# Kernel optimization log

Hardware: AMD Instinct MI355X
Metric: run time of the kernel (lower is better)

## Reference

```python
import jax, jax.numpy as jnp
import numpy as np

EMBED = 1024
HEADS = 16
HEAD_DIM = EMBED // HEADS
EPS = 1e-5  # torch LayerNorm default


def setup_inputs() -> dict:
    key = jax.random.key(0)
    ks = jax.random.split(key, 11)
    s = 1.0 / np.sqrt(EMBED)
    def lin(kw, kb):
        W = jax.random.uniform(kw, (EMBED, EMBED), jnp.float32, -s, s)
        b = jax.random.uniform(kb, (EMBED,), jnp.float32, -s, s)
        return W, b
    Wq, bq = lin(ks[0], ks[1])
    Wk, bk = lin(ks[2], ks[3])
    Wv, bv = lin(ks[4], ks[5])
    Wo, bo = lin(ks[6], ks[7])
    x = jax.random.normal(ks[8], (2, 2048, EMBED), jnp.float32)
    gamma = jnp.ones((EMBED,), jnp.float32)
    beta = jnp.zeros((EMBED,), jnp.float32)
    return {"x": x, "Wq": Wq, "bq": bq, "Wk": Wk, "bk": bk,
            "Wv": Wv, "bv": bv, "Wo": Wo, "bo": bo,
            "gamma": gamma, "beta": beta}


def _attn(x, Wq, bq, Wk, bk, Wv, bv, Wo, bo, gamma, beta):
    N, S, _ = x.shape
    # torch Linear: y = x @ W.T + b
    q = (x @ Wq.T + bq).reshape(N, S, HEADS, HEAD_DIM).transpose(0, 2, 1, 3)
    k = (x @ Wk.T + bk).reshape(N, S, HEADS, HEAD_DIM).transpose(0, 2, 1, 3)
    v = (x @ Wv.T + bv).reshape(N, S, HEADS, HEAD_DIM).transpose(0, 2, 1, 3)
    energy = jnp.einsum("bhqd,bhkd->bhqk", q, k) / np.sqrt(HEAD_DIM)
    causal = jnp.tril(jnp.ones((S, S), bool))  # [S,S]
    energy = jnp.where(causal[None, None], energy, -jnp.inf)
    attn = jax.nn.softmax(energy, axis=-1)
    out = jnp.einsum("bhqk,bhkd->bhqd", attn, v)
    out = out.transpose(0, 2, 1, 3).reshape(N, S, EMBED)
    out = out @ Wo.T + bo
    # residual + LayerNorm
    h = out + x
    mu = jnp.mean(h, axis=-1, keepdims=True)
    var = jnp.var(h, axis=-1, keepdims=True)
    return (h - mu) * jax.lax.rsqrt(var + EPS) * gamma + beta


def reference(x, Wq, bq, Wk, bk, Wv, bv, Wo, bo, gamma, beta):
    return _attn(x, Wq, bq, Wk, bk, Wv, bv, Wo, bo, gamma, beta)
```

## Files before the change

### kernel.cpp

```cpp
#include <hip/hip_runtime.h>

typedef __attribute__((ext_vector_type(8))) short short8;
typedef __attribute__((ext_vector_type(4))) float f32x4;
typedef __attribute__((ext_vector_type(4))) short short4v;

template<bool B> struct BoolC { static constexpr bool value = B; };

__device__ __forceinline__ short f2bs(float f) {
    union { float f; unsigned u; } c; c.f = f;
    unsigned r = 0x7FFFu + ((c.u >> 16) & 1u);
    return (short)((c.u + r) >> 16);
}

__device__ __forceinline__ float bs2f(short s) {
    union { unsigned u; float f; } c; c.u = ((unsigned)(unsigned short)s) << 16;
    return c.f;
}

__device__ __forceinline__ unsigned fbits(float f) {
    union { float f; unsigned u; } c; c.f = f; return c.u;
}

__device__ __forceinline__ float fast_exp2(float x) {
    float r;
    asm("v_exp_f32 %0, %1" : "=v"(r) : "v"(x));
    return r;
}

__device__ __forceinline__ void gld_lds16(const void* g, void* l) {
    __builtin_amdgcn_global_load_lds(
        (const __attribute__((address_space(1))) unsigned int*)g,
        (__attribute__((address_space(3))) unsigned int*)l, 16, 0, 0);
}

__device__ __forceinline__ f32x4 mfma16(short8 a, short8 b, f32x4 c) {
    return __builtin_amdgcn_mfma_f32_16x16x32_bf16(a, b, c, 0, 0, 0);
}

template<int N> __device__ __forceinline__ void vmwait() {
    if constexpr (N == 0)      asm volatile("s_waitcnt vmcnt(0)" ::: "memory");
    else if constexpr (N == 3) asm volatile("s_waitcnt vmcnt(3)" ::: "memory");
    else if constexpr (N == 4) asm volatile("s_waitcnt vmcnt(4)" ::: "memory");
}

__global__ __launch_bounds__(256) void cvtall_kernel(
    const float* __restrict__ x,
    const float* __restrict__ Wq, const float* __restrict__ Wk,
    const float* __restrict__ Wv, const float* __restrict__ Wo,
    short* __restrict__ xb, short* __restrict__ wqkv, short* __restrict__ wob)
{
    int i = blockIdx.x * 256 + threadIdx.x;
    const float* src; short* dst; int off;
    if (i < 1048576) { src = x; dst = xb; off = i; }
    else {
        int j = i - 1048576, which = j >> 18;
        off = j & 262143;
        src = which == 0 ? Wq : (which == 1 ? Wk : (which == 2 ? Wv : Wo));
        dst = which == 3 ? wob : (wqkv + (size_t)which * 1048576);
    }
    float4 v = ((const float4*)src)[off];
    short4v o;
    o.x = f2bs(v.x); o.y = f2bs(v.y); o.z = f2bs(v.z); o.w = f2bs(v.w);
    ((short4v*)dst)[off] = o;
}

#define BK 32

template<int MODE, int BMt, int BNt, int NTHR>
__global__ __launch_bounds__(NTHR) void gemm_bt(
    const short* __restrict__ A, const short* __restrict__ B,
    int M, int N, int K,
    const float* __restrict__ b0, const float* __restrict__ b1, const float* __restrict__ b2,
    short* __restrict__ oq, short* __restrict__ ok_, short* __restrict__ ov,
    const float* __restrict__ bo, const float* __restrict__ xres,
    short* __restrict__ outh)
{
    constexpr int WCOLS = BNt / 64;
    constexpr int IM = BMt / 2 / 16;
    constexpr int BUFSZ = (BMt + BNt) * BK;
    __shared__ __align__(16) short SM[3 * BUFSZ];
    const int tid = threadIdx.x;
    const int wave = tid >> 6, lane = tid & 63;
    const int lhi = lane >> 4, llo = lane & 15;
    const int row0 = blockIdx.x * BMt, col0 = blockIdx.y * BNt;
    const int wr = (wave / WCOLS) * (BMt / 2);
    const int wc = (wave % WCOLS) * 64;

    f32x4 acc[IM][4] = {};

    const short* gA0 = A + (size_t)(row0 + (tid >> 2)) * K + (tid & 3) * 8;
    const short* gB0 = B + (size_t)(col0 + (tid >> 2)) * K + (tid & 3) * 8;
    const short* gB1 = B + (size_t)(col0 + NTHR / 4 + (tid >> 2)) * K + (tid & 3) * 8;

    auto stage = [&](int kk, int bf) {
        short* As = SM + bf * BUFSZ;
        short* Bs = As + BMt * BK;
        gld_lds16(gA0 + kk, &As[wave * 512]);
        gld_lds16(gB0 + kk, &Bs[wave * 512]);
        gld_lds16(gB1 + kk, &Bs[NTHR * 8 + wave * 512]);
    };

    const int NT = K / BK;
    stage(0, 0);
    stage(BK, 1);

    for (int kt = 0; kt < NT; ++kt) {
        if (kt < NT - 1) vmwait<3>(); else vmwait<0>();
        __builtin_amdgcn_s_barrier();
        __builtin_amdgcn_sched_barrier(0);
        if (kt + 2 < NT) stage((kt + 2) * BK, (kt + 2) % 3);
        const short* As = SM + (kt % 3) * BUFSZ;
        const short* Bs = As + BMt * BK;
        short8 af[IM], bfr[4];
        #pragma unroll
        for (int i = 0; i < IM; ++i)
            af[i] = *(const short8*)&As[(wr + i * 16 + llo) * BK + lhi * 8];
        #pragma unroll
        for (int j = 0; j < 4; ++j)
            bfr[j] = *(const short8*)&Bs[(wc + j * 16 + llo) * BK + lhi * 8];
        #pragma unroll
        for (int i = 0; i < IM; ++i)
            #pragma unroll
            for (int j = 0; j < 4; ++j)
                acc[i][j] = mfma16(af[i], bfr[j], acc[i][j]);
    }

    if constexpr (MODE == 0) {
        const int which = col0 >> 10;
        if (which < 2) {
            const float* bia = which == 0 ? b0 : b1;
            short* dst = which == 0 ? oq : ok_;
            #pragma unroll
            for (int i = 0; i < IM; ++i)
                #pragma unroll
                for (int j = 0; j < 4; ++j)
                    #pragma unroll
                    for (int r = 0; r < 4; ++r) {
                        int m = row0 + wr + i * 16 + lhi * 4 + r;
                        int nn = (col0 & 1023) + wc + j * 16 + llo;
                        float v = acc[i][j][r] + bia[nn];
                        int h = nn >> 6, d = nn & 63;
                        int bb = m >> 11, s = m & 2047;
                        dst[((size_t)((bb * 16 + h) * 2048 + s)) * 64 + d] = f2bs(v);
                    }
        } else {
            __syncthreads();
            short* T = SM + wave * (64 * 26);
            const int nn0 = (col0 - 2048) + wc;
            const int h = nn0 >> 6;
            const int bb = row0 >> 11;
            const int s0 = (row0 & 2047) + wr;
            short* vdst = ov + ((size_t)(bb * 16 + h) * 64) * 2048;
            #pragma unroll
            for (int i = 0; i < IM; ++i) {
                #pragma unroll
                for (int j = 0; j < 4; ++j) {
                    const float bias = b2[nn0 + j * 16 + llo];
                    unsigned u01 = __builtin_amdgcn_perm(fbits(acc[i][j][1] + bias),
                                                         fbits(acc[i][j][0] + bias), 0x07060302u);
                    unsigned u23 = __builtin_amdgcn_perm(fbits(acc[i][j][3] + bias),
                                                         fbits(acc[i][j][2] + bias), 0x07060302u);
                    unsigned* Tw = (unsigned*)&T[(j * 16 + llo) * 26];
                    Tw[lhi * 2]     = u01;
                    Tw[lhi * 2 + 1] = u23;
                }
                short8 a0 = *(const short8*)&T[lane * 26];
                short8 a1 = *(const short8*)&T[lane * 26 + 8];
                *(short8*)&vdst[(size_t)lane * 2048 + s0 + i * 16]     = a0;
                *(short8*)&vdst[(size_t)lane * 2048 + s0 + i * 16 + 8] = a1;
            }
        }
    } else {
        #pragma unroll
        for (int i = 0; i < IM; ++i)
            #pragma unroll
            for (int j = 0; j < 4; ++j)
                #pragma unroll
                for (int r = 0; r < 4; ++r) {
                    int m = row0 + wr + i * 16 + lhi * 4 + r;
                    int n = col0 + wc + j * 16 + llo;
                    size_t idx = (size_t)m * N + n;
                    outh[idx] = f2bs(acc[i][j][r] + bo[n] + xres[idx]);
                }
    }
}

#define SCL 0.18033688011f

__global__ __launch_bounds__(256) void attn_kernel(
    const short* __restrict__ Q, const short* __restrict__ K,
    const short* __restrict__ Vt, short* __restrict__ O)
{
    const int id = blockIdx.x;
    const int u = id >> 3;
    const int bh = (id & 7) * 4 + (u & 3);
    const int s4 = u >> 2;
    const int p = (s4 < 8) ? (2 * s4) : (31 - 2 * s4);
    const int q0L = p * 64, q0H = (31 - p) * 64;
    const int ntH = 32 - p;

    const short* Qb = Q  + (size_t)bh * 2048 * 64;
    const short* Kb = K  + (size_t)bh * 2048 * 64;
    const short* Vb = Vt + (size_t)bh * 64 * 2048;

    __shared__ __align__(16) short Ks[2][64 * 64];
    __shared__ __align__(16) short Vs[2][64 * 64];
    __shared__ __align__(16) short Ps[4][2][16 * 68];

    const int tid = threadIdx.x, wave = tid >> 6, lane = tid & 63;
    const int lhi = lane >> 4, llo = lane & 15;
    const int qwL = q0L + wave * 16, qwH = q0H + wave * 16;
    const int qgL = qwL + llo, qgH = qwH + llo;

    auto scale8 = [](short8 a) {
        short8 r;
        #pragma unroll
        for (int i = 0; i < 8; ++i) {
            union { unsigned u; float f; } c; c.u = ((unsigned)(unsigned short)a[i]) << 16;
            r[i] = f2bs(c.f * SCL);
        }
        return r;
    };
    const short8 qfL0 = scale8(*(const short8*)&Qb[(size_t)(qwL + llo) * 64 + lhi * 8]);
    const short8 qfL1 = scale8(*(const short8*)&Qb[(size_t)(qwL + llo) * 64 + 32 + lhi * 8]);
    const short8 qfH0 = scale8(*(const short8*)&Qb[(size_t)(qwH + llo) * 64 + lhi * 8]);
    const short8 qfH1 = scale8(*(const short8*)&Qb[(size_t)(qwH + llo) * 64 + 32 + lhi * 8]);

    const int tr = tid >> 3, tc = tid & 7, sc = tc ^ (tr & 7);
    const short* kS0 = Kb + (size_t)tr * 64 + sc * 8;
    const short* kS1 = Kb + (size_t)(32 + tr) * 64 + sc * 8;
    const short* vS0 = Vb + (size_t)tr * 2048 + sc * 8;
    const short* vS1 = Vb + (size_t)(32 + tr) * 2048 + sc * 8;
    const int dOff = wave * 512;

    f32x4 oL[4] = {}, oH[4] = {};
    float lL = 0.f, lH = 0.f;

    unsigned* PwH = (unsigned*)Ps[wave][0] + llo * 34;
    unsigned* PwL = (unsigned*)Ps[wave][1] + llo * 34;

    gld_lds16(kS0, Ks[0] + dOff);
    gld_lds16(kS1, Ks[0] + 2048 + dOff);
    gld_lds16(vS0, Vs[0] + dOff);
    gld_lds16(vS1, Vs[0] + 2048 + dOff);
    __syncthreads();

    const int swq = (llo & 7) << 3;

    auto smx = [&](f32x4 (&st)[4], float& lrow, unsigned* Pw, int qg, int kk0, bool diag) {
        if (diag) {
            #pragma unroll
            for (int t = 0; t < 4; ++t)
                #pragma unroll
                for (int j = 0; j < 4; ++j)
                    if (kk0 + t * 16 + lhi * 4 + j > qg) st[t][j] = -1e30f;
        }
        float rs0 = 0.f, rs1 = 0.f;
        #pragma unroll
        for (int t = 0; t < 4; ++t) {
            st[t][0] = fast_exp2(st[t][0]);
            st[t][1] = fast_exp2(st[t][1]);
            st[t][2] = fast_exp2(st[t][2]);
            st[t][3] = fast_exp2(st[t][3]);
            rs0 += st[t][0] + st[t][2];
            rs1 += st[t][1] + st[t][3];
        }
        lrow += rs0 + rs1;
        #pragma unroll
        for (int t = 0; t < 4; ++t) {
            uint2 w;
            w.x = __builtin_amdgcn_perm(fbits(st[t][1]), fbits(st[t][0]), 0x07060302u);
            w.y = __builtin_amdgcn_perm(fbits(st[t][3]), fbits(st[t][2]), 0x07060302u);
            *(uint2*)&Pw[t * 8 + lhi * 2] = w;
        }
    };

    int cur = 0;
    auto tile = [&](int kt, auto dualc) {
        constexpr bool DUAL = decltype(dualc)::value;
        const int kk0 = kt * 64;
        if (kt + 1 < ntH) {
            const int nk = kk0 + 64;
            gld_lds16(kS0 + (size_t)nk * 64, Ks[cur ^ 1] + dOff);
            gld_lds16(kS1 + (size_t)nk * 64, Ks[cur ^ 1] + 2048 + dOff);
            gld_lds16(vS0 + nk, Vs[cur ^ 1] + dOff);
            gld_lds16(vS1 + nk, Vs[cur ^ 1] + 2048 + dOff);
        }

        f32x4 stH[4], stL[4];
        __builtin_amdgcn_s_setprio(1);
        #pragma unroll
        for (int t = 0; t < 4; ++t) {
            const int row = t * 16 + llo;
            short8 kf0 = *(const short8*)&Ks[cur][row * 64 + ((lhi * 8) ^ swq)];
            short8 kf1 = *(const short8*)&Ks[cur][row * 64 + ((lhi * 8 + 32) ^ swq)];
            f32x4 a = {};
            a = mfma16(kf0, qfH0, a);
            stH[t] = mfma16(kf1, qfH1, a);
            if (DUAL) {
                f32x4 b = {};
                b = mfma16(kf0, qfL0, b);
                stL[t] = mfma16(kf1, qfL1, b);
            }
        }
        __builtin_amdgcn_s_setprio(0);

        smx(stH, lH, PwH, qgH, kk0, kt == ntH - 1);
        if (DUAL) smx(stL, lL, PwL, qgL, kk0, kt == p);

        const short8 pH0 = *(const short8*)&Ps[wave][0][llo * 68 + lhi * 8];
        const short8 pH1 = *(const short8*)&Ps[wave][0][llo * 68 + 32 + lhi * 8];
        short8 pL0, pL1;
        if (DUAL) {
            pL0 = *(const short8*)&Ps[wave][1][llo * 68 + lhi * 8];
            pL1 = *(const short8*)&Ps[wave][1][llo * 68 + 32 + lhi * 8];
        }
        __builtin_amdgcn_s_setprio(1);
        #pragma unroll
        for (int dt = 0; dt < 4; ++dt) {
            const int row = dt * 16 + llo;
            short8 vf0 = *(const short8*)&Vs[cur][row * 64 + ((lhi * 8) ^ swq)];
            short8 vf1 = *(const short8*)&Vs[cur][row * 64 + ((lhi * 8 + 32) ^ swq)];
            oH[dt] = mfma16(pH0, vf0, oH[dt]);
            oH[dt] = mfma16(pH1, vf1, oH[dt]);
            if (DUAL) {
                oL[dt] = mfma16(pL0, vf0, oL[dt]);
                oL[dt] = mfma16(pL1, vf1, oL[dt]);
            }
        }
        __builtin_amdgcn_s_setprio(0);

        if (kt + 1 < ntH) __syncthreads();
        cur ^= 1;
    };

    for (int kt = 0; kt <= p; ++kt)      tile(kt, BoolC<true>{});
    for (int kt = p + 1; kt < ntH; ++kt) tile(kt, BoolC<false>{});

    lH += __shfl_xor(lH, 16); lH += __shfl_xor(lH, 32);
    lL += __shfl_xor(lL, 16); lL += __shfl_xor(lL, 32);
    const int b = bh >> 4, h = bh & 15;
    const float invH = 1.f / lH, invL = 1.f / lL;
    #pragma unroll
    for (int j = 0; j < 4; ++j) {
        const float ivH = __shfl(invH, lhi * 4 + j);
        const float ivL = __shfl(invL, lhi * 4 + j);
        const size_t rowH = (size_t)(b * 2048 + qwH + lhi * 4 + j);
        const size_t rowL = (size_t)(b * 2048 + qwL + lhi * 4 + j);
        #pragma unroll
        for (int dt = 0; dt < 4; ++dt) {
            int d = dt * 16 + llo;
            O[rowH * 1024 + h * 64 + d] = f2bs(oH[dt][j] * ivH);
            O[rowL * 1024 + h * 64 + d] = f2bs(oL[dt][j] * ivL);
        }
    }
}

__global__ __launch_bounds__(256) void ln_kernel(const short* __restrict__ hb,
        float* __restrict__ out,
        const float* __restrict__ gamma, const float* __restrict__ beta)
{
    const int row = blockIdx.x;
    const short* pin = hb + (size_t)row * 1024;
    float* pout = out + (size_t)row * 1024;
    const int tid = threadIdx.x;
    short4v hv = ((const short4v*)pin)[tid];
    float4 v;
    v.x = bs2f(hv.x); v.y = bs2f(hv.y); v.z = bs2f(hv.z); v.w = bs2f(hv.w);
    float s = v.x + v.y + v.z + v.w;
    float ss = v.x * v.x + v.y * v.y + v.z * v.z + v.w * v.w;
    #pragma unroll
    for (int d = 1; d < 64; d <<= 1) {
        s  += __shfl_xor(s, d);
        ss += __shfl_xor(ss, d);
    }
    __shared__ float red[8];
    const int wave = tid >> 6, lane = tid & 63;
    if (lane == 0) { red[wave] = s; red[4 + wave] = ss; }
    __syncthreads();
    s  = red[0] + red[1] + red[2] + red[3];
    ss = red[4] + red[5] + red[6] + red[7];
    const float mu = s * (1.0f / 1024.0f);
    const float var = ss * (1.0f / 1024.0f) - mu * mu;
    const float rstd = rsqrtf(var + 1e-5f);
    float4 g = ((const float4*)gamma)[tid];
    float4 b = ((const float4*)beta)[tid];
    v.x = (v.x - mu) * rstd * g.x + b.x;
    v.y = (v.y - mu) * rstd * g.y + b.y;
    v.z = (v.z - mu) * rstd * g.z + b.z;
    v.w = (v.w - mu) * rstd * g.w + b.w;
    ((float4*)pout)[tid] = v;
}

extern "C" void kernel_launch(void* const* d_in, const int* in_sizes, int n_in,
                              void* d_out, int out_size, void* d_ws, size_t ws_size,
                              hipStream_t stream)
{
    const float* x  = (const float*)d_in[0];
    const float* Wq = (const float*)d_in[1];
    const float* bq = (const float*)d_in[2];
    const float* Wk = (const float*)d_in[3];
    const float* bk = (const float*)d_in[4];
    const float* Wv = (const float*)d_in[5];
    const float* bv = (const float*)d_in[6];
    const float* Wo = (const float*)d_in[7];
    const float* bo = (const float*)d_in[8];
    const float* gamma = (const float*)d_in[9];
    const float* beta  = (const float*)d_in[10];
    float* out = (float*)d_out;

    char* ws = (char*)d_ws;
    short* xb   = (short*)(ws);
    short* wqkv = (short*)(ws + (8ull  << 20));
    short* wob  = (short*)(ws + (14ull << 20));
    short* qb   = (short*)(ws + (16ull << 20));
    short* kb   = (short*)(ws + (24ull << 20));
    short* vtb  = (short*)(ws + (32ull << 20));
    short* ab   = xb;
    short* hb   = qb;

    cvtall_kernel<<<8192, 256, 0, stream>>>(x, Wq, Wk, Wv, Wo, xb, wqkv, wob);

    gemm_bt<0, 128, 256, 512><<<dim3(32, 12), 512, 0, stream>>>(xb, wqkv, 4096, 3072, 1024,
        bq, bk, bv, qb, kb, vtb, nullptr, nullptr, nullptr);

    attn_kernel<<<512, 256, 0, stream>>>(qb, kb, vtb, ab);

    gemm_bt<1, 64, 128, 256><<<dim3(64, 8), 256, 0, stream>>>(ab, wob, 4096, 1024, 1024,
        nullptr, nullptr, nullptr, nullptr, nullptr, nullptr, bo, x, hb);

    ln_kernel<<<4096, 256, 0, stream>>>(hb, out, gamma, beta);
}
```

Before: 107.5 us.

## Replace paired low/high query tiles with one query tile per block in attention

The causal attention kernel previously had each block process two 64-row query tiles (one near the start, one near the end) so that every block did the same amount of work and shared the K/V loads. It now gives each block a single query tile, launches twice as many blocks, and orders them longest-first. This makes the kernel simpler, lowers register and LDS use, and exposes more parallelism. In exchange, blocks now do uneven amounts of work and each K/V tile is loaded more times across the grid.

```diff
diff --git a/kernel.cpp b/kernel.cpp
--- a/kernel.cpp
+++ b/kernel.cpp
@@ -3,8 +3,6 @@
 typedef __attribute__((ext_vector_type(8))) short short8;
 typedef __attribute__((ext_vector_type(4))) float f32x4;
 typedef __attribute__((ext_vector_type(4))) short short4v;
-
-template<bool B> struct BoolC { static constexpr bool value = B; };
 
 __device__ __forceinline__ short f2bs(float f) {
     union { float f; unsigned u; } c; c.f = f;
@@ -192,12 +190,10 @@
     const short* __restrict__ Vt, short* __restrict__ O)
 {
     const int id = blockIdx.x;
-    const int u = id >> 3;
-    const int bh = (id & 7) * 4 + (u & 3);
-    const int s4 = u >> 2;
-    const int p = (s4 < 8) ? (2 * s4) : (31 - 2 * s4);
-    const int q0L = p * 64, q0H = (31 - p) * 64;
-    const int ntH = 32 - p;
+    const int bh = (id & 7) * 4 + (id >> 8);
+    const int qt = 31 - ((id >> 3) & 31);
+    const int q0 = qt * 64;
+    const int nt = qt + 1;
 
     const short* Qb = Q  + (size_t)bh * 2048 * 64;
     const short* Kb = K  + (size_t)bh * 2048 * 64;
@@ -205,12 +201,12 @@
 
     __shared__ __align__(16) short Ks[2][64 * 64];
     __shared__ __align__(16) short Vs[2][64 * 64];
-    __shared__ __align__(16) short Ps[4][2][16 * 68];
+    __shared__ __align__(16) short Ps[4][16 * 68];
 
     const int tid = threadIdx.x, wave = tid >> 6, lane = tid & 63;
     const int lhi = lane >> 4, llo = lane & 15;
-    const int qwL = q0L + wave * 16, qwH = q0H + wave * 16;
-    const int qgL = qwL + llo, qgH = qwH + llo;
+    const int qw = q0 + wave * 16;
+    const int qg = qw + llo;
 
     auto scale8 = [](short8 a) {
         short8 r;
@@ -221,10 +217,8 @@
         }
         return r;
     };
-    const short8 qfL0 = scale8(*(const short8*)&Qb[(size_t)(qwL + llo) * 64 + lhi * 8]);
-    const short8 qfL1 = scale8(*(const short8*)&Qb[(size_t)(qwL + llo) * 64 + 32 + lhi * 8]);
-    const short8 qfH0 = scale8(*(const short8*)&Qb[(size_t)(qwH + llo) * 64 + lhi * 8]);
-    const short8 qfH1 = scale8(*(const short8*)&Qb[(size_t)(qwH + llo) * 64 + 32 + lhi * 8]);
+    const short8 qf0 = scale8(*(const short8*)&Qb[(size_t)(qw + llo) * 64 + lhi * 8]);
+    const short8 qf1 = scale8(*(const short8*)&Qb[(size_t)(qw + llo) * 64 + 32 + lhi * 8]);
 
     const int tr = tid >> 3, tc = tid & 7, sc = tc ^ (tr & 7);
     const short* kS0 = Kb + (size_t)tr * 64 + sc * 8;
@@ -233,11 +227,10 @@
     const short* vS1 = Vb + (size_t)(32 + tr) * 2048 + sc * 8;
     const int dOff = wave * 512;
 
-    f32x4 oL[4] = {}, oH[4] = {};
-    float lL = 0.f, lH = 0.f;
-
-    unsigned* PwH = (unsigned*)Ps[wave][0] + llo * 34;
-    unsigned* PwL = (unsigned*)Ps[wave][1] + llo * 34;
+    f32x4 o[4] = {};
+    float lrow = 0.f;
+
+    unsigned* Pw = (unsigned*)Ps[wave] + llo * 34;
 
     gld_lds16(kS0, Ks[0] + dOff);
     gld_lds16(kS1, Ks[0] + 2048 + dOff);
@@ -247,14 +240,38 @@
 
     const int swq = (llo & 7) << 3;
 
-    auto smx = [&](f32x4 (&st)[4], float& lrow, unsigned* Pw, int qg, int kk0, bool diag) {
-        if (diag) {
+    int cur = 0;
+    for (int kt = 0; kt < nt; ++kt) {
+        const int kk0 = kt * 64;
+        if (kt + 1 < nt) {
+            const int nk = kk0 + 64;
+            gld_lds16(kS0 + (size_t)nk * 64, Ks[cur ^ 1] + dOff);
+            gld_lds16(kS1 + (size_t)nk * 64, Ks[cur ^ 1] + 2048 + dOff);
+            gld_lds16(vS0 + nk, Vs[cur ^ 1] + dOff);
+            gld_lds16(vS1 + nk, Vs[cur ^ 1] + 2048 + dOff);
+        }
+
+        f32x4 st[4];
+        __builtin_amdgcn_s_setprio(1);
+        #pragma unroll
+        for (int t = 0; t < 4; ++t) {
+            const int row = t * 16 + llo;
+            short8 kf0 = *(const short8*)&Ks[cur][row * 64 + ((lhi * 8) ^ swq)];
+            short8 kf1 = *(const short8*)&Ks[cur][row * 64 + ((lhi * 8 + 32) ^ swq)];
+            f32x4 a = {};
+            a = mfma16(kf0, qf0, a);
+            st[t] = mfma16(kf1, qf1, a);
+        }
+        __builtin_amdgcn_s_setprio(0);
+
+        if (kt == nt - 1) {
             #pragma unroll
             for (int t = 0; t < 4; ++t)
                 #pragma unroll
                 for (int j = 0; j < 4; ++j)
                     if (kk0 + t * 16 + lhi * 4 + j > qg) st[t][j] = -1e30f;
         }
+
         float rs0 = 0.f, rs1 = 0.f;
         #pragma unroll
         for (int t = 0; t < 4; ++t) {
@@ -273,85 +290,36 @@
             w.y = __builtin_amdgcn_perm(fbits(st[t][3]), fbits(st[t][2]), 0x07060302u);
             *(uint2*)&Pw[t * 8 + lhi * 2] = w;
         }
-    };
-
-    int cur = 0;
-    auto tile = [&](int kt, auto dualc) {
-        constexpr bool DUAL = decltype(dualc)::value;
-        const int kk0 = kt * 64;
-        if (kt + 1 < ntH) {
-            const int nk = kk0 + 64;
-            gld_lds16(kS0 + (size_t)nk * 64, Ks[cur ^ 1] + dOff);
-            gld_lds16(kS1 + (size_t)nk * 64, Ks[cur ^ 1] + 2048 + dOff);
-            gld_lds16(vS0 + nk, Vs[cur ^ 1] + dOff);
-            gld_lds16(vS1 + nk, Vs[cur ^ 1] + 2048 + dOff);
-        }
-
-        f32x4 stH[4], stL[4];
-        __builtin_amdgcn_s_setprio(1);
-        #pragma unroll
-        for (int t = 0; t < 4; ++t) {
-            const int row = t * 16 + llo;
-            short8 kf0 = *(const short8*)&Ks[cur][row * 64 + ((lhi * 8) ^ swq)];
-            short8 kf1 = *(const short8*)&Ks[cur][row * 64 + ((lhi * 8 + 32) ^ swq)];
-            f32x4 a = {};
-            a = mfma16(kf0, qfH0, a);
-            stH[t] = mfma16(kf1, qfH1, a);
-            if (DUAL) {
-                f32x4 b = {};
-                b = mfma16(kf0, qfL0, b);
-                stL[t] = mfma16(kf1, qfL1, b);
-            }
-        }
-        __builtin_amdgcn_s_setprio(0);
-
-        smx(stH, lH, PwH, qgH, kk0, kt == ntH - 1);
-        if (DUAL) smx(stL, lL, PwL, qgL, kk0, kt == p);
-
-        const short8 pH0 = *(const short8*)&Ps[wave][0][llo * 68 + lhi * 8];
-        const short8 pH1 = *(const short8*)&Ps[wave][0][llo * 68 + 32 + lhi * 8];
-        short8 pL0, pL1;
-        if (DUAL) {
-            pL0 = *(const short8*)&Ps[wave][1][llo * 68 + lhi * 8];
-            pL1 = *(const short8*)&Ps[wave][1][llo * 68 + 32 + lhi * 8];
-        }
+
+        const short8 pf0 = *(const short8*)&Ps[wave][llo * 68 + lhi * 8];
+        const short8 pf1 = *(const short8*)&Ps[wave][llo * 68 + 32 + lhi * 8];
         __builtin_amdgcn_s_setprio(1);
         #pragma unroll
         for (int dt = 0; dt < 4; ++dt) {
             const int row = dt * 16 + llo;
             short8 vf0 = *(const short8*)&Vs[cur][row * 64 + ((lhi * 8) ^ swq)];
             short8 vf1 = *(const short8*)&Vs[cur][row * 64 + ((lhi * 8 + 32) ^ swq)];
-            oH[dt] = mfma16(pH0, vf0, oH[dt]);
-            oH[dt] = mfma16(pH1, vf1, oH[dt]);
-            if (DUAL) {
-                oL[dt] = mfma16(pL0, vf0, oL[dt]);
-                oL[dt] = mfma16(pL1, vf1, oL[dt]);
-            }
+            o[dt] = mfma16(pf0, vf0, o[dt]);
+            o[dt] = mfma16(pf1, vf1, o[dt]);
         }
         __builtin_amdgcn_s_setprio(0);
 
-        if (kt + 1 < ntH) __syncthreads();
+        if (kt + 1 < nt) __syncthreads();
         cur ^= 1;
-    };
-
-    for (int kt = 0; kt <= p; ++kt)      tile(kt, BoolC<true>{});
-    for (int kt = p + 1; kt < ntH; ++kt) tile(kt, BoolC<false>{});
-
-    lH += __shfl_xor(lH, 16); lH += __shfl_xor(lH, 32);
-    lL += __shfl_xor(lL, 16); lL += __shfl_xor(lL, 32);
+    }
+
+    lrow += __shfl_xor(lrow, 16);
+    lrow += __shfl_xor(lrow, 32);
     const int b = bh >> 4, h = bh & 15;
-    const float invH = 1.f / lH, invL = 1.f / lL;
+    const float inv = 1.f / lrow;
     #pragma unroll
     for (int j = 0; j < 4; ++j) {
-        const float ivH = __shfl(invH, lhi * 4 + j);
-        const float ivL = __shfl(invL, lhi * 4 + j);
-        const size_t rowH = (size_t)(b * 2048 + qwH + lhi * 4 + j);
-        const size_t rowL = (size_t)(b * 2048 + qwL + lhi * 4 + j);
+        const float iv = __shfl(inv, lhi * 4 + j);
+        const size_t row = (size_t)(b * 2048 + qw + lhi * 4 + j);
         #pragma unroll
         for (int dt = 0; dt < 4; ++dt) {
             int d = dt * 16 + llo;
-            O[rowH * 1024 + h * 64 + d] = f2bs(oH[dt][j] * ivH);
-            O[rowL * 1024 + h * 64 + d] = f2bs(oL[dt][j] * ivL);
+            O[row * 1024 + h * 64 + d] = f2bs(o[dt][j] * iv);
         }
     }
 }
@@ -424,7 +392,7 @@
     gemm_bt<0, 128, 256, 512><<<dim3(32, 12), 512, 0, stream>>>(xb, wqkv, 4096, 3072, 1024,
         bq, bk, bv, qb, kb, vtb, nullptr, nullptr, nullptr);
 
-    attn_kernel<<<512, 256, 0, stream>>>(qb, kb, vtb, ab);
+    attn_kernel<<<1024, 256, 0, stream>>>(qb, kb, vtb, ab);
 
     gemm_bt<1, 64, 128, 256><<<dim3(64, 8), 256, 0, stream>>>(ab, wob, 4096, 1024, 1024,
         nullptr, nullptr, nullptr, nullptr, nullptr, nullptr, bo, x, hb);
```

Result: slower. 115.4 us (+7.3%).
